# Performance work log

Hardware: AMD Instinct MI355X
Metric: run time of the kernel (lower is better)

Reference implementation:

```python
import jax, jax.numpy as jnp
import numpy as np

N_NODES = 50000
N_EDGES = 800000
D_IN, D_HID, D_OUT = 64, 128, 64


def _glorot(key, fan_in, fan_out):
    lim = (6.0 / (fan_in + fan_out)) ** 0.5
    return jax.random.uniform(key, (fan_in, fan_out), jnp.float32, -lim, lim)


def setup_inputs() -> dict:
    key = jax.random.key(0)
    ks = jax.random.split(key, 10)
    x = jax.random.normal(ks[0], (N_NODES, D_IN), jnp.float32)
    edge_index = jax.random.randint(ks[1], (2, N_EDGES), 0, N_NODES, jnp.int64)
    # GINConv1 MLP: Linear(D_IN->D_HID), ReLU, Linear(D_HID->D_HID)
    W1a = _glorot(ks[2], D_IN, D_HID); b1a = jnp.zeros((D_HID,), jnp.float32)
    W1b = _glorot(ks[3], D_HID, D_HID); b1b = jnp.zeros((D_HID,), jnp.float32)
    # GINConv2 MLP: Linear(D_HID->D_HID), ReLU, Linear(D_HID->D_OUT)
    W2a = _glorot(ks[4], D_HID, D_HID); b2a = jnp.zeros((D_HID,), jnp.float32)
    W2b = _glorot(ks[5], D_HID, D_OUT); b2b = jnp.zeros((D_OUT,), jnp.float32)
    return {"x": x, "edge_index": edge_index,
            "W1a": W1a, "b1a": b1a, "W1b": W1b, "b1b": b1b,
            "W2a": W2a, "b2a": b2a, "W2b": W2b, "b2b": b2b}


def _gin_conv(x, src, dst, Wa, ba, Wb, bb):
    # GIN aggregation (eps = 0): h_i = x_i + sum_{j in N(i)} x_j
    msgs = x[src]                                   # [E, d] gather
    agg = jax.ops.segment_sum(msgs, dst, num_segments=x.shape[0])  # [N, d]
    h = x + agg
    # 2-layer MLP
    h = jax.nn.relu(h @ Wa + ba)
    return h @ Wb + bb


def reference(x, edge_index, W1a, b1a, W1b, b1b, W2a, b2a, W2b, b2b):
    src, dst = edge_index[0], edge_index[1]
    h = jax.nn.relu(_gin_conv(x, src, dst, W1a, b1a, W1b, b1b))
    h = jax.nn.relu(_gin_conv(h, src, dst, W2a, b2a, W2b, b2b))
    return h
```

## Files before the change

### kernel.cpp

```cpp
#include <hip/hip_runtime.h>

#define N_NODES 50000
#define N_EDGES 800000

typedef __attribute__((ext_vector_type(8))) short short8;
typedef __attribute__((ext_vector_type(4))) float floatx4;

static __device__ __forceinline__ unsigned short f2b(float f) {
    unsigned int u = __float_as_uint(f);
    unsigned int r = u + 0x7fffu + ((u >> 16) & 1u);
    return (unsigned short)(r >> 16);
}
static __device__ __forceinline__ unsigned int pk(float a, float b) {
    return (unsigned)f2b(a) | ((unsigned)f2b(b) << 16);
}
static __device__ __forceinline__ float blo(unsigned int u) {
    return __uint_as_float(u << 16);
}
static __device__ __forceinline__ float bhi(unsigned int u) {
    return __uint_as_float(u & 0xffff0000u);
}

__global__ void hist_rank_kernel(const int* __restrict__ dst,
                                 int* __restrict__ deg, int* __restrict__ rank,
                                 int n) {
    int i = blockIdx.x * blockDim.x + threadIdx.x;
    if (i < n) rank[i] = atomicAdd(&deg[dst[i]], 1);
}

__global__ __launch_bounds__(1024) void scanA_kernel(
    const int* __restrict__ deg, int* __restrict__ bsum, int n) {
    __shared__ int s[1024];
    const int tid = threadIdx.x;
    int i = blockIdx.x * 1024 + tid;
    s[tid] = (i < n) ? deg[i] : 0;
    __syncthreads();
    for (int d = 512; d > 0; d >>= 1) {
        if (tid < d) s[tid] += s[tid + d];
        __syncthreads();
    }
    if (tid == 0) bsum[blockIdx.x] = s[0];
}

__global__ __launch_bounds__(1024) void scanC_kernel(
    const int* __restrict__ deg, const int* __restrict__ bsum,
    int* __restrict__ off, int n) {
    __shared__ int s[1024];
    __shared__ int bpref;
    const int tid = threadIdx.x;
    if (tid == 0) {
        int p = 0;
        for (int j = 0; j < blockIdx.x; ++j) p += bsum[j];
        bpref = p;
    }
    const int i = blockIdx.x * 1024 + tid;
    const int v = (i < n) ? deg[i] : 0;
    s[tid] = v;
    __syncthreads();
    for (int d = 1; d < 1024; d <<= 1) {
        int t = (tid >= d) ? s[tid - d] : 0;
        __syncthreads();
        s[tid] += t;
        __syncthreads();
    }
    const int excl = s[tid] - v + bpref;
    if (i < n) {
        off[i] = excl;
        if (i == n - 1) off[n] = excl + v;
    }
}

__global__ void fill_kernel(const int* __restrict__ src,
                            const int* __restrict__ dst,
                            const int* __restrict__ rank,
                            const int* __restrict__ off,
                            unsigned short* __restrict__ nbr, int n) {
    int i = blockIdx.x * blockDim.x + threadIdx.x;
    if (i < n) nbr[off[dst[i]] + rank[i]] = (unsigned short)src[i];
}

__global__ __launch_bounds__(256) void prep_kernel(
    const float* __restrict__ W1a, const float* __restrict__ W1b,
    const float* __restrict__ W2a, const float* __restrict__ W2b,
    const float* __restrict__ x, unsigned short* __restrict__ W1aT,
    unsigned short* __restrict__ W1bT, unsigned short* __restrict__ W2aT,
    unsigned short* __restrict__ W2bT, unsigned short* __restrict__ xb,
    int* __restrict__ deg) {
    int i = blockIdx.x * 256 + threadIdx.x;
    if (i < 8192) {
        int n = i >> 6, k = i & 63;
        W1aT[i] = f2b(W1a[k * 128 + n]);
    } else if (i < 24576) {
        int j = i - 8192, n = j >> 7, k = j & 127;
        W1bT[j] = f2b(W1b[k * 128 + n]);
    } else if (i < 40960) {
        int j = i - 24576, n = j >> 7, k = j & 127;
        W2aT[j] = f2b(W2a[k * 128 + n]);
    } else if (i < 49152) {
        int j = i - 40960, n = j >> 7, k = j & 127;
        W2bT[j] = f2b(W2b[k * 64 + n]);
    } else if (i < 49152 + N_NODES * 16) {
        int j = i - 49152;
        float4 v = ((const float4*)x)[j];
        uint2 o;
        o.x = pk(v.x, v.y);
        o.y = pk(v.z, v.w);
        ((uint2*)xb)[j] = o;
    } else {
        int j = i - (49152 + N_NODES * 16);
        if (j < N_NODES) deg[j] = 0;
    }
}

__global__ __launch_bounds__(256) void gather1_kernel(
    const unsigned short* __restrict__ xb, const int* __restrict__ off,
    const unsigned short* __restrict__ nbr, unsigned short* __restrict__ t1,
    int n_nodes) {
    const int tid = threadIdx.x;
    const int node = blockIdx.x * 16 + (tid >> 4);
    const int c = tid & 15;
    if (node >= n_nodes) return;
    const uint2* xr = (const uint2*)xb;
    const uint2 a = xr[(size_t)node * 16 + c];
    float f0 = blo(a.x), f1 = bhi(a.x), f2 = blo(a.y), f3 = bhi(a.y);
    const int lo = off[node], hi = off[node + 1];
    int j = lo;
    for (; j + 4 <= hi; j += 4) {
        const int s0 = nbr[j], s1 = nbr[j + 1], s2 = nbr[j + 2],
                  s3 = nbr[j + 3];
        const uint2 v0 = xr[(size_t)s0 * 16 + c];
        const uint2 v1 = xr[(size_t)s1 * 16 + c];
        const uint2 v2 = xr[(size_t)s2 * 16 + c];
        const uint2 v3 = xr[(size_t)s3 * 16 + c];
        f0 += (blo(v0.x) + blo(v1.x)) + (blo(v2.x) + blo(v3.x));
        f1 += (bhi(v0.x) + bhi(v1.x)) + (bhi(v2.x) + bhi(v3.x));
        f2 += (blo(v0.y) + blo(v1.y)) + (blo(v2.y) + blo(v3.y));
        f3 += (bhi(v0.y) + bhi(v1.y)) + (bhi(v2.y) + bhi(v3.y));
    }
    for (; j < hi; ++j) {
        const uint2 v = xr[(size_t)nbr[j] * 16 + c];
        f0 += blo(v.x); f1 += bhi(v.x);
        f2 += blo(v.y); f3 += bhi(v.y);
    }
    uint2 o;
    o.x = pk(f0, f1);
    o.y = pk(f2, f3);
    ((uint2*)t1)[(size_t)node * 16 + c] = o;
}

__global__ __launch_bounds__(256) void gather2_kernel(
    const unsigned short* __restrict__ h, const int* __restrict__ off,
    const unsigned short* __restrict__ nbr, unsigned short* __restrict__ t2,
    int n_nodes) {
    const int tid = threadIdx.x;
    const int node = blockIdx.x * 16 + (tid >> 4);
    const int c = tid & 15;
    if (node >= n_nodes) return;
    const uint4* hr = (const uint4*)h;
    const uint4 a = hr[(size_t)node * 16 + c];
    float f0 = blo(a.x), f1 = bhi(a.x), f2 = blo(a.y), f3 = bhi(a.y);
    float f4 = blo(a.z), f5 = bhi(a.z), f6 = blo(a.w), f7 = bhi(a.w);
    const int lo = off[node], hi = off[node + 1];
    int j = lo;
    for (; j + 4 <= hi; j += 4) {
        const int s0 = nbr[j], s1 = nbr[j + 1], s2 = nbr[j + 2],
                  s3 = nbr[j + 3];
        const uint4 v0 = hr[(size_t)s0 * 16 + c];
        const uint4 v1 = hr[(size_t)s1 * 16 + c];
        const uint4 v2 = hr[(size_t)s2 * 16 + c];
        const uint4 v3 = hr[(size_t)s3 * 16 + c];
        f0 += (blo(v0.x) + blo(v1.x)) + (blo(v2.x) + blo(v3.x));
        f1 += (bhi(v0.x) + bhi(v1.x)) + (bhi(v2.x) + bhi(v3.x));
        f2 += (blo(v0.y) + blo(v1.y)) + (blo(v2.y) + blo(v3.y));
        f3 += (bhi(v0.y) + bhi(v1.y)) + (bhi(v2.y) + bhi(v3.y));
        f4 += (blo(v0.z) + blo(v1.z)) + (blo(v2.z) + blo(v3.z));
        f5 += (bhi(v0.z) + bhi(v1.z)) + (bhi(v2.z) + bhi(v3.z));
        f6 += (blo(v0.w) + blo(v1.w)) + (blo(v2.w) + blo(v3.w));
        f7 += (bhi(v0.w) + bhi(v1.w)) + (bhi(v2.w) + bhi(v3.w));
    }
    for (; j < hi; ++j) {
        const uint4 v = hr[(size_t)nbr[j] * 16 + c];
        f0 += blo(v.x); f1 += bhi(v.x); f2 += blo(v.y); f3 += bhi(v.y);
        f4 += blo(v.z); f5 += bhi(v.z); f6 += blo(v.w); f7 += bhi(v.w);
    }
    uint4 o;
    o.x = pk(f0, f1); o.y = pk(f2, f3);
    o.z = pk(f4, f5); o.w = pk(f6, f7);
    ((uint4*)t2)[(size_t)node * 16 + c] = o;
}

template <int DIN, int DH, int DOUT, bool OUT_BF16>
__global__ __launch_bounds__(256) void mlp_mfma_kernel(
    const unsigned short* __restrict__ t, const unsigned short* __restrict__ WaT,
    const float* __restrict__ ba, const unsigned short* __restrict__ WbT,
    const float* __restrict__ bb, void* __restrict__ outp, int n_rows) {
    constexpr int SA = DIN + 16;
    constexpr int SH = DH + 16;
    __shared__ unsigned short tA[64 * SA];
    __shared__ unsigned short hidA[64 * SH];

    const int tid = threadIdx.x;
    const int row0 = blockIdx.x * 64;

    constexpr int CHUNKS = 64 * DIN / 8;
    const uint4* tg = (const uint4*)t;
    for (int i = tid; i < CHUNKS; i += 256) {
        const int row = i / (DIN / 8);
        const int cb = i % (DIN / 8);
        uint4 v = {0u, 0u, 0u, 0u};
        const int gr = row0 + row;
        if (gr < n_rows) v = tg[(size_t)gr * (DIN / 8) + cb];
        *(uint4*)&tA[row * SA + cb * 8] = v;
    }
    __syncthreads();

    const int lane = tid & 63;
    const int wv = tid >> 6;
    const int quad = lane >> 4;
    const int l16 = lane & 15;
    const int m0 = wv * 16;

    short8 a1[DIN / 32];
#pragma unroll
    for (int kk = 0; kk < DIN / 32; ++kk)
        a1[kk] = *(const short8*)&tA[(m0 + l16) * SA + kk * 32 + quad * 8];
#pragma unroll
    for (int nt = 0; nt < DH / 16; ++nt) {
        floatx4 acc = {0.f, 0.f, 0.f, 0.f};
#pragma unroll
        for (int kk = 0; kk < DIN / 32; ++kk) {
            short8 b =
                *(const short8*)&WaT[(nt * 16 + l16) * DIN + kk * 32 + quad * 8];
            acc = __builtin_amdgcn_mfma_f32_16x16x32_bf16(a1[kk], b, acc, 0, 0, 0);
        }
        const float bias = ba[nt * 16 + l16];
#pragma unroll
        for (int r = 0; r < 4; ++r) {
            const float v = fmaxf(acc[r] + bias, 0.f);
            hidA[(m0 + quad * 4 + r) * SH + nt * 16 + l16] = f2b(v);
        }
    }

    short8 a2[DH / 32];
#pragma unroll
    for (int kk = 0; kk < DH / 32; ++kk)
        a2[kk] = *(const short8*)&hidA[(m0 + l16) * SH + kk * 32 + quad * 8];
#pragma unroll
    for (int nt = 0; nt < DOUT / 16; ++nt) {
        floatx4 acc = {0.f, 0.f, 0.f, 0.f};
#pragma unroll
        for (int kk = 0; kk < DH / 32; ++kk) {
            short8 b =
                *(const short8*)&WbT[(nt * 16 + l16) * DH + kk * 32 + quad * 8];
            acc = __builtin_amdgcn_mfma_f32_16x16x32_bf16(a2[kk], b, acc, 0, 0, 0);
        }
        const float bias = bb[nt * 16 + l16];
#pragma unroll
        for (int r = 0; r < 4; ++r) {
            const float v = fmaxf(acc[r] + bias, 0.f);
            const int grow = row0 + m0 + quad * 4 + r;
            if (grow < n_rows) {
                if (OUT_BF16)
                    ((unsigned short*)outp)[(size_t)grow * DOUT + nt * 16 + l16] =
                        f2b(v);
                else
                    ((float*)outp)[(size_t)grow * DOUT + nt * 16 + l16] = v;
            }
        }
    }
}

extern "C" void kernel_launch(void* const* d_in, const int* in_sizes, int n_in,
                              void* d_out, int out_size, void* d_ws,
                              size_t ws_size, hipStream_t stream) {
    const float* x   = (const float*)d_in[0];
    const int*   ei  = (const int*)d_in[1];
    const float* W1a = (const float*)d_in[2];
    const float* b1a = (const float*)d_in[3];
    const float* W1b = (const float*)d_in[4];
    const float* b1b = (const float*)d_in[5];
    const float* W2a = (const float*)d_in[6];
    const float* b2a = (const float*)d_in[7];
    const float* W2b = (const float*)d_in[8];
    const float* b2b = (const float*)d_in[9];
    float* out = (float*)d_out;

    const int* src = ei;
    const int* dst = ei + N_EDGES;

    unsigned short* xb = (unsigned short*)d_ws;
    unsigned short* t1 = xb + (size_t)N_NODES * 64;
    unsigned short* h  = t1 + (size_t)N_NODES * 64;
    unsigned short* t2 = h + (size_t)N_NODES * 128;
    unsigned short* W1aT = t2 + (size_t)N_NODES * 128;
    unsigned short* W1bT = W1aT + 8192;
    unsigned short* W2aT = W1bT + 16384;
    unsigned short* W2bT = W2aT + 16384;
    int* deg  = (int*)(W2bT + 8192);
    int* off  = deg + N_NODES;
    int* bsum = off + N_NODES + 1;
    int* rank = bsum + 64;
    unsigned short* nbr = (unsigned short*)(rank + N_EDGES);

    constexpr int NB = (N_NODES + 1023) / 1024;
    constexpr int PREP_THREADS = 49152 + N_NODES * 16 + N_NODES;

    prep_kernel<<<(PREP_THREADS + 255) / 256, 256, 0, stream>>>(
        W1a, W1b, W2a, W2b, x, W1aT, W1bT, W2aT, W2bT, xb, deg);

    hist_rank_kernel<<<(N_EDGES + 255) / 256, 256, 0, stream>>>(dst, deg, rank,
                                                                N_EDGES);
    scanA_kernel<<<NB, 1024, 0, stream>>>(deg, bsum, N_NODES);
    scanC_kernel<<<NB, 1024, 0, stream>>>(deg, bsum, off, N_NODES);
    fill_kernel<<<(N_EDGES + 255) / 256, 256, 0, stream>>>(src, dst, rank, off,
                                                           nbr, N_EDGES);

    gather1_kernel<<<(N_NODES + 15) / 16, 256, 0, stream>>>(xb, off, nbr, t1,
                                                            N_NODES);
    mlp_mfma_kernel<64, 128, 128, true>
        <<<(N_NODES + 63) / 64, 256, 0, stream>>>(t1, W1aT, b1a, W1bT, b1b, h,
                                                  N_NODES);

    gather2_kernel<<<(N_NODES + 15) / 16, 256, 0, stream>>>(h, off, nbr, t2,
                                                            N_NODES);
    mlp_mfma_kernel<128, 128, 64, false>
        <<<(N_NODES + 63) / 64, 256, 0, stream>>>(t2, W2aT, b2a, W2bT, b2b, out,
                                                  N_NODES);
}
```

Baseline: 239.4 us.

## Fuse neighbor gather into MLP kernel and broadcast neighbor indices via shuffles

```diff
diff --git a/kernel.cpp b/kernel.cpp
--- a/kernel.cpp
+++ b/kernel.cpp
@@ -112,105 +112,115 @@
     }
 }
 
-__global__ __launch_bounds__(256) void gather1_kernel(
-    const unsigned short* __restrict__ xb, const int* __restrict__ off,
-    const unsigned short* __restrict__ nbr, unsigned short* __restrict__ t1,
-    int n_nodes) {
-    const int tid = threadIdx.x;
-    const int node = blockIdx.x * 16 + (tid >> 4);
-    const int c = tid & 15;
-    if (node >= n_nodes) return;
-    const uint2* xr = (const uint2*)xb;
-    const uint2 a = xr[(size_t)node * 16 + c];
-    float f0 = blo(a.x), f1 = bhi(a.x), f2 = blo(a.y), f3 = bhi(a.y);
-    const int lo = off[node], hi = off[node + 1];
-    int j = lo;
-    for (; j + 4 <= hi; j += 4) {
-        const int s0 = nbr[j], s1 = nbr[j + 1], s2 = nbr[j + 2],
-                  s3 = nbr[j + 3];
-        const uint2 v0 = xr[(size_t)s0 * 16 + c];
-        const uint2 v1 = xr[(size_t)s1 * 16 + c];
-        const uint2 v2 = xr[(size_t)s2 * 16 + c];
-        const uint2 v3 = xr[(size_t)s3 * 16 + c];
-        f0 += (blo(v0.x) + blo(v1.x)) + (blo(v2.x) + blo(v3.x));
-        f1 += (bhi(v0.x) + bhi(v1.x)) + (bhi(v2.x) + bhi(v3.x));
-        f2 += (blo(v0.y) + blo(v1.y)) + (blo(v2.y) + blo(v3.y));
-        f3 += (bhi(v0.y) + bhi(v1.y)) + (bhi(v2.y) + bhi(v3.y));
-    }
-    for (; j < hi; ++j) {
-        const uint2 v = xr[(size_t)nbr[j] * 16 + c];
-        f0 += blo(v.x); f1 += bhi(v.x);
-        f2 += blo(v.y); f3 += bhi(v.y);
-    }
-    uint2 o;
-    o.x = pk(f0, f1);
-    o.y = pk(f2, f3);
-    ((uint2*)t1)[(size_t)node * 16 + c] = o;
-}
-
-__global__ __launch_bounds__(256) void gather2_kernel(
-    const unsigned short* __restrict__ h, const int* __restrict__ off,
-    const unsigned short* __restrict__ nbr, unsigned short* __restrict__ t2,
-    int n_nodes) {
-    const int tid = threadIdx.x;
-    const int node = blockIdx.x * 16 + (tid >> 4);
-    const int c = tid & 15;
-    if (node >= n_nodes) return;
-    const uint4* hr = (const uint4*)h;
-    const uint4 a = hr[(size_t)node * 16 + c];
-    float f0 = blo(a.x), f1 = bhi(a.x), f2 = blo(a.y), f3 = bhi(a.y);
-    float f4 = blo(a.z), f5 = bhi(a.z), f6 = blo(a.w), f7 = bhi(a.w);
-    const int lo = off[node], hi = off[node + 1];
-    int j = lo;
-    for (; j + 4 <= hi; j += 4) {
-        const int s0 = nbr[j], s1 = nbr[j + 1], s2 = nbr[j + 2],
-                  s3 = nbr[j + 3];
-        const uint4 v0 = hr[(size_t)s0 * 16 + c];
-        const uint4 v1 = hr[(size_t)s1 * 16 + c];
-        const uint4 v2 = hr[(size_t)s2 * 16 + c];
-        const uint4 v3 = hr[(size_t)s3 * 16 + c];
-        f0 += (blo(v0.x) + blo(v1.x)) + (blo(v2.x) + blo(v3.x));
-        f1 += (bhi(v0.x) + bhi(v1.x)) + (bhi(v2.x) + bhi(v3.x));
-        f2 += (blo(v0.y) + blo(v1.y)) + (blo(v2.y) + blo(v3.y));
-        f3 += (bhi(v0.y) + bhi(v1.y)) + (bhi(v2.y) + bhi(v3.y));
-        f4 += (blo(v0.z) + blo(v1.z)) + (blo(v2.z) + blo(v3.z));
-        f5 += (bhi(v0.z) + bhi(v1.z)) + (bhi(v2.z) + bhi(v3.z));
-        f6 += (blo(v0.w) + blo(v1.w)) + (blo(v2.w) + blo(v3.w));
-        f7 += (bhi(v0.w) + bhi(v1.w)) + (bhi(v2.w) + bhi(v3.w));
-    }
-    for (; j < hi; ++j) {
-        const uint4 v = hr[(size_t)nbr[j] * 16 + c];
-        f0 += blo(v.x); f1 += bhi(v.x); f2 += blo(v.y); f3 += bhi(v.y);
-        f4 += blo(v.z); f5 += bhi(v.z); f6 += blo(v.w); f7 += bhi(v.w);
-    }
-    uint4 o;
-    o.x = pk(f0, f1); o.y = pk(f2, f3);
-    o.z = pk(f4, f5); o.w = pk(f6, f7);
-    ((uint4*)t2)[(size_t)node * 16 + c] = o;
-}
-
 template <int DIN, int DH, int DOUT, bool OUT_BF16>
-__global__ __launch_bounds__(256) void mlp_mfma_kernel(
-    const unsigned short* __restrict__ t, const unsigned short* __restrict__ WaT,
-    const float* __restrict__ ba, const unsigned short* __restrict__ WbT,
-    const float* __restrict__ bb, void* __restrict__ outp, int n_rows) {
+__global__ __launch_bounds__(256) void gin_fused_kernel(
+    const unsigned short* __restrict__ xin, const int* __restrict__ off,
+    const unsigned short* __restrict__ nbr,
+    const unsigned short* __restrict__ WaT, const float* __restrict__ ba,
+    const unsigned short* __restrict__ WbT, const float* __restrict__ bb,
+    void* __restrict__ outp, int n_rows) {
     constexpr int SA = DIN + 16;
     constexpr int SH = DH + 16;
-    __shared__ unsigned short tA[64 * SA];
-    __shared__ unsigned short hidA[64 * SH];
+    __shared__ __attribute__((aligned(16))) unsigned short tA[64 * SA];
+    __shared__ __attribute__((aligned(16))) unsigned short hidA[64 * SH];
 
     const int tid = threadIdx.x;
     const int row0 = blockIdx.x * 64;
-
-    constexpr int CHUNKS = 64 * DIN / 8;
-    const uint4* tg = (const uint4*)t;
-    for (int i = tid; i < CHUNKS; i += 256) {
-        const int row = i / (DIN / 8);
-        const int cb = i % (DIN / 8);
-        uint4 v = {0u, 0u, 0u, 0u};
-        const int gr = row0 + row;
-        if (gr < n_rows) v = tg[(size_t)gr * (DIN / 8) + cb];
-        *(uint4*)&tA[row * SA + cb * 8] = v;
+    const int grp = tid >> 4;
+    const int c = tid & 15;
+
+    for (int t = 0; t < 4; ++t) {
+        const int r = grp * 4 + t;
+        const int node = row0 + r;
+        if (DIN == 64) {
+            float f0 = 0.f, f1 = 0.f, f2 = 0.f, f3 = 0.f;
+            if (node < n_rows) {
+                const uint2* xr = (const uint2*)xin;
+                const uint2 a = xr[(size_t)node * 16 + c];
+                f0 = blo(a.x); f1 = bhi(a.x); f2 = blo(a.y); f3 = bhi(a.y);
+                const int lo = off[node], hi = off[node + 1];
+                int j = lo;
+                while (j < hi) {
+                    const int rem = hi - j;
+                    const int nch = rem < 16 ? rem : 16;
+                    const int myidx = (c < nch) ? (int)nbr[j + c] : 0;
+                    int k = 0;
+                    for (; k + 4 <= nch; k += 4) {
+                        const int s0 = __shfl(myidx, k, 16);
+                        const int s1 = __shfl(myidx, k + 1, 16);
+                        const int s2 = __shfl(myidx, k + 2, 16);
+                        const int s3 = __shfl(myidx, k + 3, 16);
+                        const uint2 v0 = xr[(size_t)s0 * 16 + c];
+                        const uint2 v1 = xr[(size_t)s1 * 16 + c];
+                        const uint2 v2 = xr[(size_t)s2 * 16 + c];
+                        const uint2 v3 = xr[(size_t)s3 * 16 + c];
+                        f0 += (blo(v0.x) + blo(v1.x)) + (blo(v2.x) + blo(v3.x));
+                        f1 += (bhi(v0.x) + bhi(v1.x)) + (bhi(v2.x) + bhi(v3.x));
+                        f2 += (blo(v0.y) + blo(v1.y)) + (blo(v2.y) + blo(v3.y));
+                        f3 += (bhi(v0.y) + bhi(v1.y)) + (bhi(v2.y) + bhi(v3.y));
+                    }
+                    for (; k < nch; ++k) {
+                        const int s = __shfl(myidx, k, 16);
+                        const uint2 v = xr[(size_t)s * 16 + c];
+                        f0 += blo(v.x); f1 += bhi(v.x);
+                        f2 += blo(v.y); f3 += bhi(v.y);
+                    }
+                    j += nch;
+                }
+            }
+            uint2 o;
+            o.x = pk(f0, f1);
+            o.y = pk(f2, f3);
+            *(uint2*)&tA[r * SA + c * 4] = o;
+        } else {
+            float f0 = 0.f, f1 = 0.f, f2 = 0.f, f3 = 0.f;
+            float f4 = 0.f, f5 = 0.f, f6 = 0.f, f7 = 0.f;
+            if (node < n_rows) {
+                const uint4* hr = (const uint4*)xin;
+                const uint4 a = hr[(size_t)node * 16 + c];
+                f0 = blo(a.x); f1 = bhi(a.x); f2 = blo(a.y); f3 = bhi(a.y);
+                f4 = blo(a.z); f5 = bhi(a.z); f6 = blo(a.w); f7 = bhi(a.w);
+                const int lo = off[node], hi = off[node + 1];
+                int j = lo;
+                while (j < hi) {
+                    const int rem = hi - j;
+                    const int nch = rem < 16 ? rem : 16;
+                    const int myidx = (c < nch) ? (int)nbr[j + c] : 0;
+                    int k = 0;
+                    for (; k + 4 <= nch; k += 4) {
+                        const int s0 = __shfl(myidx, k, 16);
+                        const int s1 = __shfl(myidx, k + 1, 16);
+                        const int s2 = __shfl(myidx, k + 2, 16);
+                        const int s3 = __shfl(myidx, k + 3, 16);
+                        const uint4 v0 = hr[(size_t)s0 * 16 + c];
+                        const uint4 v1 = hr[(size_t)s1 * 16 + c];
+                        const uint4 v2 = hr[(size_t)s2 * 16 + c];
+                        const uint4 v3 = hr[(size_t)s3 * 16 + c];
+                        f0 += (blo(v0.x) + blo(v1.x)) + (blo(v2.x) + blo(v3.x));
+                        f1 += (bhi(v0.x) + bhi(v1.x)) + (bhi(v2.x) + bhi(v3.x));
+                        f2 += (blo(v0.y) + blo(v1.y)) + (blo(v2.y) + blo(v3.y));
+                        f3 += (bhi(v0.y) + bhi(v1.y)) + (bhi(v2.y) + bhi(v3.y));
+                        f4 += (blo(v0.z) + blo(v1.z)) + (blo(v2.z) + blo(v3.z));
+                        f5 += (bhi(v0.z) + bhi(v1.z)) + (bhi(v2.z) + bhi(v3.z));
+                        f6 += (blo(v0.w) + blo(v1.w)) + (blo(v2.w) + blo(v3.w));
+                        f7 += (bhi(v0.w) + bhi(v1.w)) + (bhi(v2.w) + bhi(v3.w));
+                    }
+                    for (; k < nch; ++k) {
+                        const int s = __shfl(myidx, k, 16);
+                        const uint4 v = hr[(size_t)s * 16 + c];
+                        f0 += blo(v.x); f1 += bhi(v.x);
+                        f2 += blo(v.y); f3 += bhi(v.y);
+                        f4 += blo(v.z); f5 += bhi(v.z);
+                        f6 += blo(v.w); f7 += bhi(v.w);
+                    }
+                    j += nch;
+                }
+            }
+            uint4 o;
+            o.x = pk(f0, f1); o.y = pk(f2, f3);
+            o.z = pk(f4, f5); o.w = pk(f6, f7);
+            *(uint4*)&tA[r * SA + c * 8] = o;
+        }
     }
     __syncthreads();
 
@@ -289,10 +299,8 @@
     const int* dst = ei + N_EDGES;
 
     unsigned short* xb = (unsigned short*)d_ws;
-    unsigned short* t1 = xb + (size_t)N_NODES * 64;
-    unsigned short* h  = t1 + (size_t)N_NODES * 64;
-    unsigned short* t2 = h + (size_t)N_NODES * 128;
-    unsigned short* W1aT = t2 + (size_t)N_NODES * 128;
+    unsigned short* h  = xb + (size_t)N_NODES * 64;
+    unsigned short* W1aT = h + (size_t)N_NODES * 128;
     unsigned short* W1bT = W1aT + 8192;
     unsigned short* W2aT = W1bT + 16384;
     unsigned short* W2bT = W2aT + 16384;
@@ -315,15 +323,11 @@
     fill_kernel<<<(N_EDGES + 255) / 256, 256, 0, stream>>>(src, dst, rank, off,
                                                            nbr, N_EDGES);
 
-    gather1_kernel<<<(N_NODES + 15) / 16, 256, 0, stream>>>(xb, off, nbr, t1,
-                                                            N_NODES);
-    mlp_mfma_kernel<64, 128, 128, true>
-        <<<(N_NODES + 63) / 64, 256, 0, stream>>>(t1, W1aT, b1a, W1bT, b1b, h,
-                                                  N_NODES);
-
-    gather2_kernel<<<(N_NODES + 15) / 16, 256, 0, stream>>>(h, off, nbr, t2,
-                                                            N_NODES);
-    mlp_mfma_kernel<128, 128, 64, false>
-        <<<(N_NODES + 63) / 64, 256, 0, stream>>>(t2, W2aT, b2a, W2bT, b2b, out,
-                                                  N_NODES);
-}
+    gin_fused_kernel<64, 128, 128, true>
+        <<<(N_NODES + 63) / 64, 256, 0, stream>>>(xb, off, nbr, W1aT, b1a, W1bT,
+                                                  b1b, h, N_NODES);
+
+    gin_fused_kernel<128, 128, 64, false>
+        <<<(N_NODES + 63) / 64, 256, 0, stream>>>(h, off, nbr, W2aT, b2a, W2bT,
+                                                  b2b, out, N_NODES);
+}
```

Result: no change. 237.0 us (-1.0%).
